# Optimization experiments

Hardware: AMD Instinct MI355X
Metric: run time of the kernel (lower is better)

The kernel has to match this reference:

```python
import jax, jax.numpy as jnp
import numpy as np

B, T, C = 2, 2048, 2048
NH = 16          # n_head
G = 4            # group_size
NKV = NH // G    # kv heads
HD = C // NH     # head_dim = 128
BASE = 10000.0


def setup_inputs() -> dict:
    key = jax.random.key(0)
    ks = jax.random.split(key, 9)
    s = 0.02
    return {
        "x": jax.random.normal(ks[0], (B, T, C), jnp.float32),
        "wq_w": jax.random.normal(ks[1], (C, C), jnp.float32) * s,
        "wq_b": jax.random.normal(ks[2], (C,), jnp.float32) * s,
        "wk_w": jax.random.normal(ks[3], (C // G, C), jnp.float32) * s,
        "wk_b": jax.random.normal(ks[4], (C // G,), jnp.float32) * s,
        "wv_w": jax.random.normal(ks[5], (C // G, C), jnp.float32) * s,
        "wv_b": jax.random.normal(ks[6], (C // G,), jnp.float32) * s,
        "cp_w": jax.random.normal(ks[7], (C, C), jnp.float32) * s,
        "cp_b": jax.random.normal(ks[8], (C,), jnp.float32) * s,
    }


def _rope(x):
    # Faithful to source: RoPE is applied to [B, H, T, HD] but the module
    # reads seq_len = x.size(1) == H, so the rotation angle is indexed by the
    # HEAD axis and broadcast over sequence positions.
    b, h, t, d = x.shape
    half = d // 2
    theta = 1.0 / (BASE ** (jnp.arange(0, half, dtype=jnp.float32) * 2.0 / d))  # [half]
    ang = jnp.arange(h, dtype=jnp.float32)[:, None] * theta[None, :]            # [h, half]
    cos = jnp.cos(ang)[None, :, None, :]  # [1, h, 1, half]
    sin = jnp.sin(ang)[None, :, None, :]
    xs = x.reshape(b, h, t, half, 2)
    x0, x1 = xs[..., 0], xs[..., 1]
    out = jnp.stack([x0 * cos - x1 * sin, x1 * cos + x0 * sin], axis=-1)
    return out.reshape(b, h, t, d)


def reference(x, wq_w, wq_b, wk_w, wk_b, wv_w, wv_b, cp_w, cp_b):
    b, t, c = x.shape
    q = x @ wq_w.T + wq_b                                  # [B,T,C]
    k = x @ wk_w.T + wk_b                                  # [B,T,C//G]
    v = x @ wv_w.T + wv_b                                  # [B,T,C//G]
    q = q.reshape(b, t, NH, HD).transpose(0, 2, 1, 3)      # [B,NH,T,HD]
    k = k.reshape(b, t, NKV, HD).transpose(0, 2, 1, 3)     # [B,NKV,T,HD]
    v = v.reshape(b, t, NKV, HD).transpose(0, 2, 1, 3)
    q = _rope(q)
    k = _rope(k)
    # GQA expand: each kv head repeated G times consecutively
    k = jnp.repeat(k, G, axis=1)                           # [B,NH,T,HD]
    v = jnp.repeat(v, G, axis=1)
    att = jnp.einsum('bhqd,bhkd->bhqk', q, k) / (HD ** 0.5)
    mask = jnp.tril(jnp.ones((t, t), dtype=bool))
    att = jnp.where(mask[None, None], att, -jnp.inf)
    att = jax.nn.softmax(att, axis=-1)
    y = jnp.einsum('bhqk,bhkd->bhqd', att, v)
    y = y.transpose(0, 2, 1, 3).reshape(b, t, c)
    return y @ cp_w.T + cp_b
```

## Files before the change

kernel.cpp:

```cpp
#include <hip/hip_runtime.h>

typedef unsigned short u16;
typedef __bf16 bf16x8 __attribute__((ext_vector_type(8)));
typedef float f32x4 __attribute__((ext_vector_type(4)));
typedef float f32x16 __attribute__((ext_vector_type(16)));
typedef unsigned u32x4 __attribute__((ext_vector_type(4)));

#define T_   2048
#define C_   2048
#define HD_  128
#define NH_  16
#define NKV_ 4
#define M_   4096

typedef __attribute__((address_space(1))) const void* as1_cvp;
typedef __attribute__((address_space(3))) void* as3_vp;

__device__ __forceinline__ void gload16(const void* g, void* l) {
  __builtin_amdgcn_global_load_lds((as1_cvp)g, (as3_vp)l, 16, 0, 0);
}

__device__ __forceinline__ u16 f2bf(float f) {
  unsigned u = __builtin_bit_cast(unsigned, f);
  return (u16)((u + 0x7fffu + ((u >> 16) & 1u)) >> 16);
}

__device__ __forceinline__ float fexp2(float x) {
  float r;
  asm("v_exp_f32 %0, %1" : "=v"(r) : "v"(x));
  return r;
}

__device__ __forceinline__ unsigned cvtpk(float a, float b) {
  unsigned d;
  asm("v_cvt_pk_bf16_f32 %0, %1, %2" : "=v"(d) : "v"(a), "v"(b));
  return d;
}

__global__ void cvt_bf16(const float4* __restrict__ in, ushort4* __restrict__ out, int n4) {
  int i = blockIdx.x * blockDim.x + threadIdx.x;
  if (i >= n4) return;
  float4 v = in[i];
  ushort4 r;
  r.x = f2bf(v.x); r.y = f2bf(v.y); r.z = f2bf(v.z); r.w = f2bf(v.w);
  out[i] = r;
}

__global__ void copy_f32(const float* __restrict__ in, float* __restrict__ out, int n) {
  int i = blockIdx.x * blockDim.x + threadIdx.x;
  if (i < n) out[i] = in[i];
}

__global__ void rope_fold_w(const float* __restrict__ W, u16* __restrict__ out, int npair) {
  int idx = blockIdx.x * blockDim.x + threadIdx.x;
  int p  = idx >> 9;
  int c4 = (idx & 511) << 2;
  if (p >= npair) return;
  int h  = p >> 6;
  int ii = p & 63;
  float theta = __expf(-(float)ii * (9.210340371976184f / 64.0f));
  float s, c;
  __sincosf((float)h * theta, &s, &c);
  size_t r0 = (size_t)(2 * p) * 2048 + c4;
  size_t r1 = r0 + 2048;
  float4 a = *(const float4*)(W + r0);
  float4 b = *(const float4*)(W + r1);
  ushort4 o0, o1;
  o0.x = f2bf(a.x * c - b.x * s); o0.y = f2bf(a.y * c - b.y * s);
  o0.z = f2bf(a.z * c - b.z * s); o0.w = f2bf(a.w * c - b.w * s);
  o1.x = f2bf(b.x * c + a.x * s); o1.y = f2bf(b.y * c + a.y * s);
  o1.z = f2bf(b.z * c + a.z * s); o1.w = f2bf(b.w * c + a.w * s);
  *(ushort4*)(out + r0) = o0;
  *(ushort4*)(out + r1) = o1;
}

__global__ void rope_fold_b(const float* __restrict__ bin, float* __restrict__ bout, int npair) {
  int p = blockIdx.x * blockDim.x + threadIdx.x;
  if (p >= npair) return;
  int h = p >> 6, ii = p & 63;
  float theta = __expf(-(float)ii * (9.210340371976184f / 64.0f));
  float s, c;
  __sincosf((float)h * theta, &s, &c);
  float a = bin[2 * p], b = bin[2 * p + 1];
  bout[2 * p]     = a * c - b * s;
  bout[2 * p + 1] = b * c + a * s;
}

template<int MODE, int NPX>
__global__ __launch_bounds__(256)
void gemm_t(const u16* __restrict__ A, const u16* __restrict__ W,
            const float* __restrict__ bias, void* __restrict__ op0,
            void* __restrict__ op1, void* __restrict__ op2, const float qscale) {
  __shared__ __align__(16) u16 sm[3 * 8192];
  const int tid  = threadIdx.x;
  const int lane = tid & 63;
  const int wr = (tid >> 6) >> 1, wc = (tid >> 6) & 1;
  const int bid = blockIdx.x;
  const int xcd = bid & 7;
  const int idx = bid >> 3;
  const int mN  = idx / NPX;
  const int nl  = idx - mN * NPX;
  const int m0  = mN << 7;
  const int n0  = (xcd * NPX + nl) << 7;
  const int K = C_;

  const int srow = tid >> 2;
  const int sch  = (tid & 3) ^ ((srow >> 1) & 3);
  const u16* gA = A + (size_t)(m0 + srow) * K + sch * 8;
  const u16* gW = W + (size_t)(n0 + srow) * K + sch * 8;
  const int ldst = srow * 32 + (tid & 3) * 8;

  const int fr = lane & 15;
  const int g  = lane >> 4;

  f32x4 acc[4][4] = {};

#define STAGE(s, k0)                                          \
  {                                                           \
    u16* base_ = sm + (s) * 8192;                             \
    gload16(gA + (k0),            base_ + ldst);              \
    gload16(gA + (k0) + 64 * K,   base_ + 64 * 32 + ldst);    \
    gload16(gW + (k0),            base_ + 4096 + ldst);       \
    gload16(gW + (k0) + 64 * K,   base_ + 4096 + 64 * 32 + ldst); \
  }

  STAGE(0, 0)
  STAGE(1, 32)
  asm volatile("s_waitcnt vmcnt(4)" ::: "memory");
  __builtin_amdgcn_s_barrier();

  int slot = 0;
  for (int kt = 0; kt < 64; ++kt) {
    int s2 = slot + 2; if (s2 >= 3) s2 -= 3;
    if (kt < 62) STAGE(s2, (kt + 2) * 32)

    const u16* bufA = sm + slot * 8192;
    const u16* bufB = bufA + 4096;
    bf16x8 af[4], bq[4];
#pragma unroll
    for (int mi = 0; mi < 4; ++mi) {
      const int row = wr * 64 + mi * 16 + fr;
      af[mi] = *(const bf16x8*)&bufA[row * 32 + ((g ^ ((row >> 1) & 3)) << 3)];
    }
#pragma unroll
    for (int ni = 0; ni < 4; ++ni) {
      const int row = wc * 64 + ni * 16 + fr;
      bq[ni] = *(const bf16x8*)&bufB[row * 32 + ((g ^ ((row >> 1) & 3)) << 3)];
    }
#pragma unroll
    for (int mi = 0; mi < 4; ++mi)
#pragma unroll
      for (int ni = 0; ni < 4; ++ni)
        acc[mi][ni] = __builtin_amdgcn_mfma_f32_16x16x32_bf16(af[mi], bq[ni], acc[mi][ni], 0, 0, 0);

    __builtin_amdgcn_sched_barrier(0);
    if (kt < 62) asm volatile("s_waitcnt vmcnt(4) lgkmcnt(0)" ::: "memory");
    else         asm volatile("s_waitcnt vmcnt(0) lgkmcnt(0)" ::: "memory");
    __builtin_amdgcn_s_barrier();
    __builtin_amdgcn_sched_barrier(0);
    slot = (slot == 2) ? 0 : slot + 1;
  }
#undef STAGE

  const int rbase = m0 + wr * 64 + ((lane >> 4) << 2);
#pragma unroll
  for (int ni = 0; ni < 4; ++ni) {
    const int cg = n0 + wc * 64 + ni * 16 + fr;
    const float bb = bias[cg];
#pragma unroll
    for (int mi = 0; mi < 4; ++mi) {
      const int rg0 = rbase + mi * 16;
#pragma unroll
      for (int r = 0; r < 4; ++r) {
        float v = acc[mi][ni][r] + bb;
        const int rg = rg0 + r;
        if (MODE == 1) {
          ((float*)op0)[(size_t)rg * C_ + cg] = v;
        } else {
          const int b = rg >> 11, t = rg & (T_ - 1);
          if (cg < 2048) {
            const int h = cg >> 7, d = cg & 127;
            ((u16*)op0)[((((size_t)b * NH_ + h) * T_ + t) << 7) + d] = f2bf(v * qscale);
          } else if (cg < 2560) {
            const int c2 = cg - 2048, h = c2 >> 7, d = c2 & 127;
            ((u16*)op1)[((((size_t)b * NKV_ + h) * T_ + t) << 7) + d] = f2bf(v);
          } else {
            const int c2 = cg - 2560, h = c2 >> 7, d = c2 & 127;
            ((u16*)op2)[(((size_t)b * NKV_ + h) * HD_ + d) * T_ + t] = f2bf(v);
          }
        }
      }
    }
  }
}

__device__ __forceinline__ void stage_kv(u16* dst, const u16* __restrict__ kg,
                                         const u16* __restrict__ vg, int lane, int w) {
#pragma unroll
  for (int r = 0; r < 4; ++r) {
    const int row = r * 16 + w * 4 + (lane >> 4);
    const int cg  = (lane & 15) ^ (row & 7);
    gload16(kg + (size_t)row * 128 + cg * 8, dst + row * 128 + (lane & 15) * 8);
  }
#pragma unroll
  for (int r = 0; r < 4; ++r) {
    const int row = r * 32 + w * 8 + (lane >> 3);
    const int cg  = (lane & 7) ^ (row & 7);
    gload16(vg + (size_t)row * T_ + cg * 8, dst + 8192 + row * 64 + (lane & 7) * 8);
  }
}

__global__ __launch_bounds__(256, 2)
void attn2(const u16* __restrict__ q, const u16* __restrict__ k,
           const u16* __restrict__ vt, u16* __restrict__ y) {
  __shared__ __align__(16) u16 sm[32768];
  const int tid  = threadIdx.x;
  const int lane = tid & 63;
  const int w    = tid >> 6;
  const int hi   = lane >> 5;
  const int l5   = lane & 31;
  const int h = blockIdx.y;
  const int b = blockIdx.z;
  const int qt = b ? (int)blockIdx.x : (15 - (int)blockIdx.x);
  const int q0  = qt << 7;
  const int q0w = q0 + w * 32;
  const int nkv = 2 * qt + 2;
  const size_t qbase = (((size_t)b * NH_ + h) * T_ + q0) * HD_;
  const size_t kbase = ((size_t)b * NKV_ + (h >> 2)) * (size_t)T_ * HD_;
  const size_t vbase = ((size_t)b * NKV_ + (h >> 2)) * (size_t)HD_ * T_;

#pragma unroll
  for (int r = 0; r < 8; ++r) {
    const int row = r * 16 + w * 4 + (lane >> 4);
    const int cg  = (lane & 15) ^ (row & 7);
    gload16(q + qbase + (size_t)row * 128 + cg * 8, sm + row * 128 + (lane & 15) * 8);
  }
  __syncthreads();
  bf16x8 qf[8];
  {
    const int row = w * 32 + l5;
#pragma unroll
    for (int kd = 0; kd < 8; ++kd)
      qf[kd] = *(const bf16x8*)&sm[row * 128 + ((((kd << 1) | hi) ^ (row & 7)) << 3)];
  }
  __syncthreads();
  stage_kv(sm, k + kbase, vt + vbase, lane, w);

  f32x16 o[4] = {};
  float m = -1e30f, l = 0.f;

  for (int kv = 0; kv < nkv; ++kv) {
    __syncthreads();
    const int buf = kv & 1;
    if (kv + 1 < nkv)
      stage_kv(sm + ((buf ^ 1) << 14),
               k + kbase + ((size_t)(kv + 1) << 6) * 128,
               vt + vbase + ((kv + 1) << 6), lane, w);

    if ((kv << 6) <= q0w + 31) {
      const u16* Ks = sm + (buf << 14);
      const u16* Vs = Ks + 8192;

      f32x16 st[2] = {};
      __builtin_amdgcn_s_setprio(1);
#pragma unroll
      for (int kt = 0; kt < 2; ++kt) {
        const int krow = kt * 32 + l5;
#pragma unroll
        for (int kd = 0; kd < 8; ++kd) {
          bf16x8 ka = *(const bf16x8*)&Ks[krow * 128 + ((((kd << 1) | hi) ^ (l5 & 7)) << 3)];
          st[kt] = __builtin_amdgcn_mfma_f32_32x32x16_bf16(ka, qf[kd], st[kt], 0, 0, 0);
        }
      }
      __builtin_amdgcn_s_setprio(0);

      if ((kv << 6) + 63 > q0w) {
        const int qg = q0w + l5;
#pragma unroll
        for (int kt = 0; kt < 2; ++kt)
#pragma unroll
          for (int r = 0; r < 16; ++r) {
            const int kg = (kv << 6) + kt * 32 + (r & 3) + ((r >> 2) << 3) + (hi << 2);
            if (kg > qg) st[kt][r] = -3.0e38f;
          }
      }

      float pmax = -3.0e38f;
#pragma unroll
      for (int kt = 0; kt < 2; ++kt)
#pragma unroll
        for (int r = 0; r < 16; ++r) pmax = fmaxf(pmax, st[kt][r]);
      pmax = fmaxf(pmax, __shfl_xor(pmax, 32));
      if (!__all(pmax - m <= 8.0f)) {
        const float mn = fmaxf(m, pmax);
        const float f = fexp2(m - mn);
        m = mn;
        l *= f;
#pragma unroll
        for (int r = 0; r < 16; ++r) {
          const float fr = __shfl(f, (r & 3) + ((r >> 2) << 3) + (hi << 2));
          o[0][r] *= fr; o[1][r] *= fr; o[2][r] *= fr; o[3][r] *= fr;
        }
      }

      float rs = 0.f;
#pragma unroll
      for (int kt = 0; kt < 2; ++kt) {
#pragma unroll
        for (int s = 0; s < 2; ++s) {
          float e0 = fexp2(st[kt][8 * s + 0] - m), e1 = fexp2(st[kt][8 * s + 1] - m);
          float e2 = fexp2(st[kt][8 * s + 2] - m), e3 = fexp2(st[kt][8 * s + 3] - m);
          float e4 = fexp2(st[kt][8 * s + 4] - m), e5 = fexp2(st[kt][8 * s + 5] - m);
          float e6 = fexp2(st[kt][8 * s + 6] - m), e7 = fexp2(st[kt][8 * s + 7] - m);
          rs += ((e0 + e1) + (e2 + e3)) + ((e4 + e5) + (e6 + e7));
          const unsigned wL0 = cvtpk(e0, e1), wL1 = cvtpk(e2, e3);
          const unsigned wH0 = cvtpk(e4, e5), wH1 = cvtpk(e6, e7);
          const unsigned s0 = hi ? wL0 : wH0, s1 = hi ? wL1 : wH1;
          const unsigned r0 = __shfl_xor(s0, 32), r1 = __shfl_xor(s1, 32);
          u32x4 fw;
          fw.x = hi ? r0 : wL0; fw.y = hi ? r1 : wL1;
          fw.z = hi ? wH0 : r0; fw.w = hi ? wH1 : r1;
          const bf16x8 pa = __builtin_bit_cast(bf16x8, fw);
          const int ch = (((kt * 2 + s) << 1) | hi) ^ (l5 & 7);
          __builtin_amdgcn_s_setprio(1);
#pragma unroll
          for (int ds = 0; ds < 4; ++ds) {
            const int vrow = ds * 32 + l5;
            bf16x8 vb = *(const bf16x8*)&Vs[vrow * 64 + (ch << 3)];
            o[ds] = __builtin_amdgcn_mfma_f32_32x32x16_bf16(pa, vb, o[ds], 0, 0, 0);
          }
          __builtin_amdgcn_s_setprio(0);
        }
      }
      rs += __shfl_xor(rs, 32);
      l += rs;
    }
  }

  const float linv = 1.0f / l;
#pragma unroll
  for (int r = 0; r < 16; ++r) {
    const int crow = (r & 3) + ((r >> 2) << 3) + (hi << 2);
    const float lf = __shfl(linv, crow);
    const int qg = q0w + crow;
    const size_t rowoff = (((size_t)(b << 11) + qg) << 11) + (h << 7) + l5;
#pragma unroll
    for (int ds = 0; ds < 4; ++ds)
      y[rowoff + ds * 32] = f2bf(o[ds][r] * lf);
  }
}

extern "C" void kernel_launch(void* const* d_in, const int* in_sizes, int n_in,
                              void* d_out, int out_size, void* d_ws, size_t ws_size,
                              hipStream_t stream) {
  (void)in_sizes; (void)n_in; (void)out_size; (void)ws_size;
  const float* x    = (const float*)d_in[0];
  const float* wq_w = (const float*)d_in[1];
  const float* wq_b = (const float*)d_in[2];
  const float* wk_w = (const float*)d_in[3];
  const float* wk_b = (const float*)d_in[4];
  const float* wv_w = (const float*)d_in[5];
  const float* wv_b = (const float*)d_in[6];
  const float* cp_w = (const float*)d_in[7];
  const float* cp_b = (const float*)d_in[8];

  char* ws = (char*)d_ws;
  u16* xb  = (u16*)ws;  ws += (size_t)M_ * C_ * 2;
  u16* wqr = (u16*)ws;  ws += (size_t)C_ * C_ * 2;
  u16* wkr = (u16*)ws;  ws += (size_t)512 * C_ * 2;
  u16* wvb = (u16*)ws;  ws += (size_t)512 * C_ * 2;
  u16* cpb = (u16*)ws;  ws += (size_t)C_ * C_ * 2;
  u16* qb  = (u16*)ws;  ws += (size_t)M_ * C_ * 2;
  u16* kb  = (u16*)ws;  ws += (size_t)M_ * 512 * 2;
  u16* vtb = (u16*)ws;  ws += (size_t)M_ * 512 * 2;
  float* bqkv = (float*)ws; ws += 3072 * 4;
  u16* yb = xb;

  cvt_bf16<<<8192, 256, 0, stream>>>((const float4*)x,    (ushort4*)xb,  2097152);
  cvt_bf16<<<1024, 256, 0, stream>>>((const float4*)wv_w, (ushort4*)wvb, 262144);
  cvt_bf16<<<4096, 256, 0, stream>>>((const float4*)cp_w, (ushort4*)cpb, 1048576);
  rope_fold_w<<<2048, 256, 0, stream>>>(wq_w, wqr, 1024);
  rope_fold_w<<<512,  256, 0, stream>>>(wk_w, wkr, 256);
  rope_fold_b<<<4, 256, 0, stream>>>(wq_b, bqkv, 1024);
  rope_fold_b<<<1, 256, 0, stream>>>(wk_b, bqkv + 2048, 256);
  copy_f32<<<2, 256, 0, stream>>>(wv_b, bqkv + 2560, 512);

  const float qscale = 0.08838834764831843f * 1.4426950408889634f;
  gemm_t<0, 3><<<768, 256, 0, stream>>>(xb, wqr, bqkv, qb, kb, vtb, qscale);

  attn2<<<dim3(16, 16, 2), 256, 0, stream>>>(qb, kb, vtb, yb);

  gemm_t<1, 2><<<512, 256, 0, stream>>>(yb, cpb, cp_b, (float*)d_out, nullptr, nullptr, 1.0f);
}
```

Baseline: 211.3 us.

## Replace GEMM with 8-wave 256xBN tile kernel using double-buffered K=64 stages

Replaces the 128x128-tile, 4-wave GEMM (triple-buffered, K=32 stages) with a 512-thread kernel that computes 256xBN tiles (BN=192 for QKV, 128 for the output projection). It uses K=64 double-buffered LDS stages and splits prefetch of A and B around interleaved MFMA phases, with s_setprio around the MFMA blocks. The larger tiles raise arithmetic intensity and cut redundant global loads. In exchange, fewer blocks run (256 per GEMM), LDS use per block is higher, and the XCD-aware block mapping is dropped, which may lower occupancy or L2 locality.

```diff
diff --git a/kernel.cpp b/kernel.cpp
--- a/kernel.cpp
+++ b/kernel.cpp
@@ -86,112 +86,135 @@
   bout[2 * p + 1] = b * c + a * s;
 }
 
-template<int MODE, int NPX>
-__global__ __launch_bounds__(256)
-void gemm_t(const u16* __restrict__ A, const u16* __restrict__ W,
-            const float* __restrict__ bias, void* __restrict__ op0,
-            void* __restrict__ op1, void* __restrict__ op2, const float qscale) {
-  __shared__ __align__(16) u16 sm[3 * 8192];
+template<int BN, int MODE>
+__global__ __launch_bounds__(512)
+void gemm8(const u16* __restrict__ A, const u16* __restrict__ W,
+           const float* __restrict__ bias, void* __restrict__ op0,
+           void* __restrict__ op1, void* __restrict__ op2, const float qscale) {
+  constexpr int NREP = BN / 64;
+  constexpr int ASZ  = 256 * 64;
+  constexpr int BSZ  = BN * 64;
+  constexpr int BUF  = ASZ + BSZ;
+  constexpr int NB   = BSZ / 4096;
+  __shared__ __align__(16) u16 sm[2 * BUF];
   const int tid  = threadIdx.x;
   const int lane = tid & 63;
-  const int wr = (tid >> 6) >> 1, wc = (tid >> 6) & 1;
-  const int bid = blockIdx.x;
-  const int xcd = bid & 7;
-  const int idx = bid >> 3;
-  const int mN  = idx / NPX;
-  const int nl  = idx - mN * NPX;
-  const int m0  = mN << 7;
-  const int n0  = (xcd * NPX + nl) << 7;
-  const int K = C_;
-
-  const int srow = tid >> 2;
-  const int sch  = (tid & 3) ^ ((srow >> 1) & 3);
-  const u16* gA = A + (size_t)(m0 + srow) * K + sch * 8;
-  const u16* gW = W + (size_t)(n0 + srow) * K + sch * 8;
-  const int ldst = srow * 32 + (tid & 3) * 8;
-
-  const int fr = lane & 15;
-  const int g  = lane >> 4;
-
-  f32x4 acc[4][4] = {};
-
-#define STAGE(s, k0)                                          \
-  {                                                           \
-    u16* base_ = sm + (s) * 8192;                             \
-    gload16(gA + (k0),            base_ + ldst);              \
-    gload16(gA + (k0) + 64 * K,   base_ + 64 * 32 + ldst);    \
-    gload16(gW + (k0),            base_ + 4096 + ldst);       \
-    gload16(gW + (k0) + 64 * K,   base_ + 4096 + 64 * 32 + ldst); \
-  }
-
-  STAGE(0, 0)
-  STAGE(1, 32)
-  asm volatile("s_waitcnt vmcnt(4)" ::: "memory");
-  __builtin_amdgcn_s_barrier();
-
-  int slot = 0;
-  for (int kt = 0; kt < 64; ++kt) {
-    int s2 = slot + 2; if (s2 >= 3) s2 -= 3;
-    if (kt < 62) STAGE(s2, (kt + 2) * 32)
-
-    const u16* bufA = sm + slot * 8192;
-    const u16* bufB = bufA + 4096;
-    bf16x8 af[4], bq[4];
+  const int wid  = tid >> 6;
+  const int wr = wid >> 2, wc = wid & 3;
+  const int m0 = blockIdx.y << 8;
+  const int n0 = blockIdx.x * BN;
+  const int K  = C_;
+  const int fr = lane & 15, g = lane >> 4;
+
+  const u16* srcA[4]; int dstA[4];
+#pragma unroll
+  for (int i = 0; i < 4; ++i) {
+    const int idx = i * 512 + tid;
+    const int row = idx >> 3, sch = (idx & 7) ^ (row & 7);
+    srcA[i] = A + (size_t)(m0 + row) * K + sch * 8;
+    dstA[i] = idx * 8;
+  }
+  const u16* srcB[NB]; int dstB[NB];
+#pragma unroll
+  for (int i = 0; i < NB; ++i) {
+    const int idx = i * 512 + tid;
+    const int row = idx >> 3, sch = (idx & 7) ^ (row & 7);
+    srcB[i] = W + (size_t)(n0 + row) * K + sch * 8;
+    dstB[i] = ASZ + idx * 8;
+  }
+  const int swz0 = ((g     ^ (fr & 7)) << 3);
+  const int swz1 = (((4+g) ^ (fr & 7)) << 3);
+
+  f32x4 acc[8][NREP] = {};
+
+#pragma unroll
+  for (int i = 0; i < 4; ++i) gload16(srcA[i], sm + dstA[i]);
+#pragma unroll
+  for (int i = 0; i < NB; ++i) gload16(srcB[i], sm + dstB[i]);
+  __syncthreads();
+
+#define LDA(MH, SWZ) {                                                   \
+  _Pragma("unroll")                                                      \
+  for (int mi = 0; mi < 4; ++mi) {                                       \
+    const int row = wr * 128 + (MH) * 64 + mi * 16 + fr;                 \
+    af[mi] = *(const bf16x8*)&sm[base + row * 64 + (SWZ)];               \
+  } }
+#define LDB(BF, SWZ) {                                                   \
+  _Pragma("unroll")                                                      \
+  for (int ni = 0; ni < NREP; ++ni) {                                    \
+    const int row = wc * (BN / 4) + ni * 16 + fr;                        \
+    BF[ni] = *(const bf16x8*)&sm[base + ASZ + row * 64 + (SWZ)];         \
+  } }
+#define MM(MH, BF) {                                                     \
+  __builtin_amdgcn_s_setprio(1);                                         \
+  _Pragma("unroll")                                                      \
+  for (int mi = 0; mi < 4; ++mi)                                         \
+    _Pragma("unroll")                                                    \
+    for (int ni = 0; ni < NREP; ++ni)                                    \
+      acc[(MH) * 4 + mi][ni] = __builtin_amdgcn_mfma_f32_16x16x32_bf16(  \
+          af[mi], BF[ni], acc[(MH) * 4 + mi][ni], 0, 0, 0);              \
+  __builtin_amdgcn_s_setprio(0); }
+
+  for (int t = 0; t < 32; ++t) {
+    const int base = (t & 1) * BUF;
+    const int pbuf = ((t & 1) ^ 1) * BUF;
+    bf16x8 af[4], bfa[NREP], bfb[NREP];
+    if (t < 31) {
+      const int ko = (t + 1) * 64;
+#pragma unroll
+      for (int i = 0; i < 4; ++i) gload16(srcA[i] + ko, sm + pbuf + dstA[i]);
+      __builtin_amdgcn_sched_barrier(0);
+    }
+    LDA(0, swz0) LDB(bfa, swz0) MM(0, bfa)
+    __builtin_amdgcn_s_barrier();
+    if (t < 31) {
+      const int ko = (t + 1) * 64;
+#pragma unroll
+      for (int i = 0; i < NB; ++i) gload16(srcB[i] + ko, sm + pbuf + dstB[i]);
+      __builtin_amdgcn_sched_barrier(0);
+    }
+    LDA(1, swz0) MM(1, bfa)
+    __builtin_amdgcn_s_barrier();
+    LDB(bfb, swz1) LDA(0, swz1) MM(0, bfb)
+    __builtin_amdgcn_s_barrier();
+    LDA(1, swz1) MM(1, bfb)
+    __syncthreads();
+  }
+#undef LDA
+#undef LDB
+#undef MM
+
+#pragma unroll
+  for (int mh = 0; mh < 2; ++mh)
 #pragma unroll
     for (int mi = 0; mi < 4; ++mi) {
-      const int row = wr * 64 + mi * 16 + fr;
-      af[mi] = *(const bf16x8*)&bufA[row * 32 + ((g ^ ((row >> 1) & 3)) << 3)];
-    }
-#pragma unroll
-    for (int ni = 0; ni < 4; ++ni) {
-      const int row = wc * 64 + ni * 16 + fr;
-      bq[ni] = *(const bf16x8*)&bufB[row * 32 + ((g ^ ((row >> 1) & 3)) << 3)];
-    }
-#pragma unroll
-    for (int mi = 0; mi < 4; ++mi)
-#pragma unroll
-      for (int ni = 0; ni < 4; ++ni)
-        acc[mi][ni] = __builtin_amdgcn_mfma_f32_16x16x32_bf16(af[mi], bq[ni], acc[mi][ni], 0, 0, 0);
-
-    __builtin_amdgcn_sched_barrier(0);
-    if (kt < 62) asm volatile("s_waitcnt vmcnt(4) lgkmcnt(0)" ::: "memory");
-    else         asm volatile("s_waitcnt vmcnt(0) lgkmcnt(0)" ::: "memory");
-    __builtin_amdgcn_s_barrier();
-    __builtin_amdgcn_sched_barrier(0);
-    slot = (slot == 2) ? 0 : slot + 1;
-  }
-#undef STAGE
-
-  const int rbase = m0 + wr * 64 + ((lane >> 4) << 2);
-#pragma unroll
-  for (int ni = 0; ni < 4; ++ni) {
-    const int cg = n0 + wc * 64 + ni * 16 + fr;
-    const float bb = bias[cg];
-#pragma unroll
-    for (int mi = 0; mi < 4; ++mi) {
-      const int rg0 = rbase + mi * 16;
-#pragma unroll
-      for (int r = 0; r < 4; ++r) {
-        float v = acc[mi][ni][r] + bb;
-        const int rg = rg0 + r;
-        if (MODE == 1) {
-          ((float*)op0)[(size_t)rg * C_ + cg] = v;
-        } else {
-          const int b = rg >> 11, t = rg & (T_ - 1);
-          if (cg < 2048) {
-            const int h = cg >> 7, d = cg & 127;
-            ((u16*)op0)[((((size_t)b * NH_ + h) * T_ + t) << 7) + d] = f2bf(v * qscale);
-          } else if (cg < 2560) {
-            const int c2 = cg - 2048, h = c2 >> 7, d = c2 & 127;
-            ((u16*)op1)[((((size_t)b * NKV_ + h) * T_ + t) << 7) + d] = f2bf(v);
+      const int rg0 = m0 + wr * 128 + mh * 64 + mi * 16 + ((lane >> 4) << 2);
+#pragma unroll
+      for (int ni = 0; ni < NREP; ++ni) {
+        const int cg = n0 + wc * (BN / 4) + ni * 16 + fr;
+        const float bb = bias[cg];
+#pragma unroll
+        for (int r = 0; r < 4; ++r) {
+          float v = acc[mh * 4 + mi][ni][r] + bb;
+          const int rg = rg0 + r;
+          if (MODE == 1) {
+            ((float*)op0)[(size_t)rg * C_ + cg] = v;
           } else {
-            const int c2 = cg - 2560, h = c2 >> 7, d = c2 & 127;
-            ((u16*)op2)[(((size_t)b * NKV_ + h) * HD_ + d) * T_ + t] = f2bf(v);
+            const int b = rg >> 11, t = rg & (T_ - 1);
+            if (cg < 2048) {
+              const int h = cg >> 7, d = cg & 127;
+              ((u16*)op0)[((((size_t)b * NH_ + h) * T_ + t) << 7) + d] = f2bf(v * qscale);
+            } else if (cg < 2560) {
+              const int c2 = cg - 2048, h = c2 >> 7, d = c2 & 127;
+              ((u16*)op1)[((((size_t)b * NKV_ + h) * T_ + t) << 7) + d] = f2bf(v);
+            } else {
+              const int c2 = cg - 2560, h = c2 >> 7, d = c2 & 127;
+              ((u16*)op2)[(((size_t)b * NKV_ + h) * HD_ + d) * T_ + t] = f2bf(v);
+            }
           }
         }
       }
     }
-  }
 }
 
 __device__ __forceinline__ void stage_kv(u16* dst, const u16* __restrict__ kg,
@@ -386,9 +409,10 @@
   copy_f32<<<2, 256, 0, stream>>>(wv_b, bqkv + 2560, 512);
 
   const float qscale = 0.08838834764831843f * 1.4426950408889634f;
-  gemm_t<0, 3><<<768, 256, 0, stream>>>(xb, wqr, bqkv, qb, kb, vtb, qscale);
+  gemm8<192, 0><<<dim3(16, 16), 512, 0, stream>>>(xb, wqr, bqkv, qb, kb, vtb, qscale);
 
   attn2<<<dim3(16, 16, 2), 256, 0, stream>>>(qb, kb, vtb, yb);
 
-  gemm_t<1, 2><<<512, 256, 0, stream>>>(yb, cpb, cp_b, (float*)d_out, nullptr, nullptr, 1.0f);
-}
+  gemm8<128, 1><<<dim3(16, 16), 512, 0, stream>>>(yb, cpb, cp_b, (float*)d_out,
+                                                  nullptr, nullptr, 1.0f);
+}
```

Result: faster. 193.0 us (-8.7%).
